# Optimization experiments

Hardware: AMD Instinct MI355X
Metric: run time of the kernel (lower is better)

## Reference

```python
import jax, jax.numpy as jnp
import numpy as np

N_HEADS = 8  # must match init_kwargs n_heads


def _shift(x, dy, dx):
    """out[..., y, x] = x[..., y+dy, x+dx], zero-padded outside. Replaces im2col gather / col2im scatter."""
    H, W = x.shape[-2], x.shape[-1]
    py0, py1 = max(dy, 0), max(-dy, 0)
    px0, px1 = max(dx, 0), max(-dx, 0)
    xp = jnp.pad(x, [(0, 0)] * (x.ndim - 2) + [(py1, py0), (px1, px0)])
    return xp[..., py1 + dy:py1 + dy + H, px1 + dx:px1 + dx + W]


def setup_inputs() -> dict:
    key = jax.random.key(0)
    k1, k2, k3 = jax.random.split(key, 3)
    N, D, H, W = 8, 256, 128, 128
    V = jax.random.normal(k1, (N, D, H, W), dtype=jnp.float32)
    K = jax.random.normal(k2, (N, D, H, W), dtype=jnp.float32)
    Q = jax.random.normal(k3, (N, D, H, W), dtype=jnp.float32)
    mask = jnp.ones((N, 1, H, W), dtype=jnp.float32)
    return {"V": V, "K": K, "Q": Q, "ksize": 5, "dilation": 1, "mask": mask}


def reference(V, K, Q, ksize, dilation, mask):
    N, D, H, W = Q.shape
    Dv = V.shape[1]
    nh = N_HEADS
    h_dim = D // nh
    dv_h = Dv // nh
    pad = (ksize // 2) * dilation
    offsets = [(i * dilation - pad, j * dilation - pad)
               for i in range(ksize) for j in range(ksize)]  # P = ksize**2 window positions

    # per-head QK scores for each window offset: score_p = sum_c K[y+dy, x+dx] * Q[y, x]
    Qh = Q.reshape(N, nh, h_dim, H, W)
    scores = []
    for (dy, dx) in offsets:
        Ks = _shift(K, dy, dx).reshape(N, nh, h_dim, H, W)
        scores.append(jnp.sum(Ks * Qh, axis=2))  # (N, nh, H, W)
    scores = jnp.stack(scores, axis=0)  # (P, N, nh, H, W)

    # softmax over window positions (dim 2 in the torch code), then mask
    att = jax.nn.softmax(scores, axis=0)
    m = mask.reshape(N, 1, H, W)[:, 0]  # (N, H, W)
    att = att * m[None, :, None, :, :]

    # diffuse V: value at (y, x) weighted by att[p] scatters to (y+dy, x+dx) (col2im add)
    Vh = V.reshape(N, nh, dv_h, H, W)
    out = jnp.zeros((N, nh, dv_h, H, W), dtype=V.dtype)
    for p, (dy, dx) in enumerate(offsets):
        contrib = Vh * att[p][:, :, None]  # (N, nh, dv_h, H, W)
        out = out + _shift(contrib, -dy, -dx)
    return out.reshape(N, Dv, H, W)
```

## Files before the change

### kernel.cpp

```cpp
#include <hip/hip_runtime.h>
#include <hip/hip_bf16.h>

typedef __hip_bfloat16 bf16;

#define N_     8
#define NH     8
#define HD     32
#define HW     (128 * 128)
#define H_     128
#define W_     128
#define P_     25
#define TY     8
#define RG     12
#define PITCH  136
#define CH     4
#define NCH    (HD / CH)
#define NPLANE (N_ * NH * HW)

static __device__ __forceinline__ unsigned short f2bf(float f) {
  bf16 b = __float2bfloat16(f);
  return *(unsigned short*)&b;
}

__global__ __launch_bounds__(512) void attn_kernel(
    const float* __restrict__ Kp, const float* __restrict__ Qp,
    const float* __restrict__ maskp, bf16* __restrict__ att) {
  __shared__ float L[CH][RG][PITCH];

  const int tid = threadIdx.x;
  const int y0 = blockIdx.x * TY, nh = blockIdx.y;
  const int ty = tid >> 6, g = tid & 63;
  const int gy = y0 + ty, gx0 = 2 * g;
  const float* KU = Kp + (size_t)nh * (HD * HW);
  const float* QU = Qp + (size_t)nh * (HD * HW);

  const int scol = tid & 127;
  const int sr0  = tid >> 7;
  int gofs[3]; bool okr[3];
#pragma unroll
  for (int j = 0; j < 3; ++j) {
    const int ky = y0 - 2 + sr0 + 4 * j;
    okr[j] = (unsigned)ky < H_;
    gofs[j] = okr[j] ? ky * W_ + scol : 0;
  }

  if (tid < 192) {
    const int ch = tid / 48, rem = tid % 48, r = rem >> 2, c = rem & 3;
    L[ch][r][c < 2 ? c : c + 128] = 0.f;
  }

  float s[P_][2];
#pragma unroll
  for (int p = 0; p < P_; ++p) { s[p][0] = 0.f; s[p][1] = 0.f; }

  float t[3][CH];
#pragma unroll
  for (int j = 0; j < 3; ++j)
#pragma unroll
    for (int ch = 0; ch < CH; ++ch)
      t[j][ch] = okr[j] ? KU[gofs[j] + ch * HW] : 0.f;

#pragma unroll 1
  for (int kc = 0; kc < NCH; ++kc) {
    const int c0 = kc * CH;
    float q[CH][2];
#pragma unroll
    for (int ch = 0; ch < CH; ++ch) {
      float2 qv = *(const float2*)(QU + (c0 + ch) * HW + gy * W_ + gx0);
      q[ch][0] = qv.x; q[ch][1] = qv.y;
    }

    if (kc) __syncthreads();
#pragma unroll
    for (int j = 0; j < 3; ++j)
#pragma unroll
      for (int ch = 0; ch < CH; ++ch)
        L[ch][sr0 + 4 * j][scol + 2] = t[j][ch];
    __syncthreads();

    if (kc < NCH - 1) {
      const int cn = (kc + 1) * CH;
#pragma unroll
      for (int j = 0; j < 3; ++j)
#pragma unroll
        for (int ch = 0; ch < CH; ++ch)
          t[j][ch] = okr[j] ? KU[gofs[j] + (cn + ch) * HW] : 0.f;
    }

#pragma unroll
    for (int ch = 0; ch < CH; ++ch)
#pragma unroll
      for (int dyi = 0; dyi < 5; ++dyi) {
        const float* rp = &L[ch][ty + dyi][2 * g];
        float2 ra = *(const float2*)rp;
        float2 rb = *(const float2*)(rp + 2);
        float2 rc = *(const float2*)(rp + 4);
        float r[6] = {ra.x, ra.y, rb.x, rb.y, rc.x, rc.y};
#pragma unroll
        for (int dxi = 0; dxi < 5; ++dxi) {
          s[dyi * 5 + dxi][0] += r[0 + dxi] * q[ch][0];
          s[dyi * 5 + dxi][1] += r[1 + dxi] * q[ch][1];
        }
      }
  }

  float2 mv = *(const float2*)(maskp + (size_t)(nh >> 3) * HW + gy * W_ + gx0);
  float inv[2];
#pragma unroll
  for (int px = 0; px < 2; ++px) {
    float m = s[0][px];
#pragma unroll
    for (int p = 1; p < P_; ++p) m = fmaxf(m, s[p][px]);
    float sum = 0.f;
#pragma unroll
    for (int p = 0; p < P_; ++p) { float e = __expf(s[p][px] - m); s[p][px] = e; sum += e; }
    inv[px] = (px ? mv.y : mv.x) / sum;
  }
  unsigned short* A = (unsigned short*)att;
  const size_t pixbase = (size_t)nh * HW + gy * W_ + gx0;
#pragma unroll
  for (int p = 0; p < P_; ++p) {
    unsigned o = (unsigned)f2bf(s[p][0] * inv[0]) |
                 ((unsigned)f2bf(s[p][1] * inv[1]) << 16);
    *(unsigned*)(A + (size_t)p * NPLANE + pixbase) = o;
  }
}

__global__ __launch_bounds__(256) void diffuse_kernel(
    const float* __restrict__ Vp, const bf16* __restrict__ att,
    float* __restrict__ out) {
  __shared__ float L[CH][RG][PITCH];

  const int tid = threadIdx.x;
  const int y0 = blockIdx.x * TY, nh = blockIdx.y;
  const int ty = tid >> 5, g = tid & 31;
  const int gy = y0 + ty, gx0 = 4 * g;
  const float* VU = Vp + (size_t)nh * (HD * HW);
  float* OU = out + (size_t)nh * (HD * HW);

  const int scol = tid & 127;
  const int sr0  = tid >> 7;
  int gofs[6]; bool okr[6];
#pragma unroll
  for (int j = 0; j < 6; ++j) {
    const int ky = y0 - 2 + sr0 + 2 * j;
    okr[j] = (unsigned)ky < H_;
    gofs[j] = okr[j] ? ky * W_ + scol : 0;
  }

  float t[6][CH];
#pragma unroll
  for (int j = 0; j < 6; ++j)
#pragma unroll
    for (int ch = 0; ch < CH; ++ch)
      t[j][ch] = okr[j] ? VU[gofs[j] + ch * HW] : 0.f;

  const unsigned short* A = (const unsigned short*)att;
  unsigned mxl[5], mxh[5];
#pragma unroll
  for (int exi = 0; exi < 5; ++exi) {
    bool o0 = (unsigned)(gx0 + 0 + exi - 2) < W_;
    bool o1 = (unsigned)(gx0 + 1 + exi - 2) < W_;
    bool o2 = (unsigned)(gx0 + 2 + exi - 2) < W_;
    bool o3 = (unsigned)(gx0 + 3 + exi - 2) < W_;
    mxl[exi] = (o0 ? 0xFFFFu : 0u) | (o1 ? 0xFFFF0000u : 0u);
    mxh[exi] = (o2 ? 0xFFFFu : 0u) | (o3 ? 0xFFFF0000u : 0u);
  }
  uint2 wp[P_];
#pragma unroll
  for (int j = 0; j < P_; ++j) {
    const int eyi = j / 5, exi = j % 5;
    const int ys = gy + eyi - 2;
    uint2 v; v.x = 0u; v.y = 0u;
    if ((unsigned)ys < H_) {
      const size_t base = (size_t)(24 - j) * NPLANE + (size_t)nh * HW +
                          (size_t)(ys * W_) + (gx0 + exi - 2);
      if (exi == 2) {
        v = *(const uint2*)(A + base);
      } else if ((exi & 1) == 0) {
        v.x = *(const unsigned*)(A + base);
        v.y = *(const unsigned*)(A + base + 2);
      } else {
        unsigned u0 = *(const unsigned*)(A + base - 1);
        unsigned u1 = *(const unsigned*)(A + base + 1);
        unsigned u2 = *(const unsigned*)(A + base + 3);
        v.x = (u0 >> 16) | (u1 << 16);
        v.y = (u1 >> 16) | (u2 << 16);
      }
    }
    v.x &= mxl[exi]; v.y &= mxh[exi];
    wp[j] = v;
  }

  if (tid < 192) {
    const int ch = tid / 48, rem = tid % 48, r = rem >> 2, c = rem & 3;
    L[ch][r][c < 2 ? c : c + 128] = 0.f;
  }

#pragma unroll 1
  for (int kc = 0; kc < NCH; ++kc) {
    if (kc) __syncthreads();
#pragma unroll
    for (int j = 0; j < 6; ++j)
#pragma unroll
      for (int ch = 0; ch < CH; ++ch)
        L[ch][sr0 + 2 * j][scol + 2] = t[j][ch];
    __syncthreads();

    if (kc < NCH - 1) {
      const int cn = (kc + 1) * CH;
#pragma unroll
      for (int j = 0; j < 6; ++j)
#pragma unroll
        for (int ch = 0; ch < CH; ++ch)
          t[j][ch] = okr[j] ? VU[gofs[j] + (cn + ch) * HW] : 0.f;
    }

    float acc[CH][4];
#pragma unroll
    for (int ch = 0; ch < CH; ++ch)
#pragma unroll
      for (int px = 0; px < 4; ++px) acc[ch][px] = 0.f;

#pragma unroll
    for (int eyi = 0; eyi < 5; ++eyi) {
      float vr[CH][8];
#pragma unroll
      for (int ch = 0; ch < CH; ++ch) {
        const float* rp = &L[ch][ty + eyi][4 * g];
        float4 ra = *(const float4*)rp;
        float4 rb = *(const float4*)(rp + 4);
        vr[ch][0] = ra.x; vr[ch][1] = ra.y; vr[ch][2] = ra.z; vr[ch][3] = ra.w;
        vr[ch][4] = rb.x; vr[ch][5] = rb.y; vr[ch][6] = rb.z; vr[ch][7] = rb.w;
      }
#pragma unroll
      for (int exi = 0; exi < 5; ++exi) {
        const uint2 w2 = wp[eyi * 5 + exi];
        float wf[4];
        wf[0] = __uint_as_float(w2.x << 16);
        wf[1] = __uint_as_float(w2.x & 0xFFFF0000u);
        wf[2] = __uint_as_float(w2.y << 16);
        wf[3] = __uint_as_float(w2.y & 0xFFFF0000u);
#pragma unroll
        for (int ch = 0; ch < CH; ++ch)
#pragma unroll
          for (int px = 0; px < 4; ++px)
            acc[ch][px] += wf[px] * vr[ch][px + exi];
      }
    }

    const int c0 = kc * CH;
#pragma unroll
    for (int ch = 0; ch < CH; ++ch) {
      float4 o = make_float4(acc[ch][0], acc[ch][1], acc[ch][2], acc[ch][3]);
      *(float4*)(OU + (c0 + ch) * HW + gy * W_ + gx0) = o;
    }
  }
}

extern "C" void kernel_launch(void* const* d_in, const int* in_sizes, int n_in,
                              void* d_out, int out_size, void* d_ws, size_t ws_size,
                              hipStream_t stream) {
  const float* V    = (const float*)d_in[0];
  const float* K    = (const float*)d_in[1];
  const float* Q    = (const float*)d_in[2];
  const float* mask = (const float*)d_in[5];

  bf16* att = (bf16*)d_ws;

  dim3 grid(H_ / TY, N_ * NH);
  attn_kernel<<<grid, 512, 0, stream>>>(K, Q, mask, att);
  diffuse_kernel<<<grid, 256, 0, stream>>>(V, att, (float*)d_out);
}
```

Baseline: 170.5 us.

## Load K window directly from global memory in attention kernel, drop LDS staging

Measured after the change: 312.5 us. +83.3%, slower.

```diff
diff --git a/kernel.cpp b/kernel.cpp
--- a/kernel.cpp
+++ b/kernel.cpp
@@ -10,98 +10,95 @@
 #define H_     128
 #define W_     128
 #define P_     25
+#define CH     4
+#define NCH    (HD / CH)
+#define NPLANE (N_ * NH * HW)
+
 #define TY     8
 #define RG     12
 #define PITCH  136
-#define CH     4
-#define NCH    (HD / CH)
-#define NPLANE (N_ * NH * HW)
+
+#define ATY    4
 
 static __device__ __forceinline__ unsigned short f2bf(float f) {
   bf16 b = __float2bfloat16(f);
   return *(unsigned short*)&b;
 }
 
-__global__ __launch_bounds__(512) void attn_kernel(
+__global__ __launch_bounds__(256) void attn_kernel(
     const float* __restrict__ Kp, const float* __restrict__ Qp,
     const float* __restrict__ maskp, bf16* __restrict__ att) {
-  __shared__ float L[CH][RG][PITCH];
-
   const int tid = threadIdx.x;
-  const int y0 = blockIdx.x * TY, nh = blockIdx.y;
+  const int y0 = blockIdx.x * ATY, nh = blockIdx.y;
   const int ty = tid >> 6, g = tid & 63;
   const int gy = y0 + ty, gx0 = 2 * g;
   const float* KU = Kp + (size_t)nh * (HD * HW);
   const float* QU = Qp + (size_t)nh * (HD * HW);
 
-  const int scol = tid & 127;
-  const int sr0  = tid >> 7;
-  int gofs[3]; bool okr[3];
-#pragma unroll
-  for (int j = 0; j < 3; ++j) {
-    const int ky = y0 - 2 + sr0 + 4 * j;
-    okr[j] = (unsigned)ky < H_;
-    gofs[j] = okr[j] ? ky * W_ + scol : 0;
-  }
-
-  if (tid < 192) {
-    const int ch = tid / 48, rem = tid % 48, r = rem >> 2, c = rem & 3;
-    L[ch][r][c < 2 ? c : c + 128] = 0.f;
-  }
+  int rowoff[5]; bool rowok[5];
+#pragma unroll
+  for (int d = 0; d < 5; ++d) {
+    const int yy = gy + d - 2;
+    rowok[d] = (unsigned)yy < H_;
+    const int yc = yy < 0 ? 0 : (yy > H_ - 1 ? H_ - 1 : yy);
+    rowoff[d] = yc * W_;
+  }
+  const int c0 = (g == 0) ? 0 : (2 * g - 2);
+  const int c1 = 2 * g;
+  const int c2 = (g == 63) ? 124 : (2 * g + 2);
 
   float s[P_][2];
 #pragma unroll
   for (int p = 0; p < P_; ++p) { s[p][0] = 0.f; s[p][1] = 0.f; }
-
-  float t[3][CH];
-#pragma unroll
-  for (int j = 0; j < 3; ++j)
-#pragma unroll
-    for (int ch = 0; ch < CH; ++ch)
-      t[j][ch] = okr[j] ? KU[gofs[j] + ch * HW] : 0.f;
 
 #pragma unroll 1
   for (int kc = 0; kc < NCH; ++kc) {
-    const int c0 = kc * CH;
+    const int cb = kc * CH;
     float q[CH][2];
 #pragma unroll
     for (int ch = 0; ch < CH; ++ch) {
-      float2 qv = *(const float2*)(QU + (c0 + ch) * HW + gy * W_ + gx0);
+      float2 qv = *(const float2*)(QU + (cb + ch) * HW + gy * W_ + gx0);
       q[ch][0] = qv.x; q[ch][1] = qv.y;
     }
 
-    if (kc) __syncthreads();
-#pragma unroll
-    for (int j = 0; j < 3; ++j)
-#pragma unroll
-      for (int ch = 0; ch < CH; ++ch)
-        L[ch][sr0 + 4 * j][scol + 2] = t[j][ch];
-    __syncthreads();
-
-    if (kc < NCH - 1) {
-      const int cn = (kc + 1) * CH;
-#pragma unroll
-      for (int j = 0; j < 3; ++j)
-#pragma unroll
-        for (int ch = 0; ch < CH; ++ch)
-          t[j][ch] = okr[j] ? KU[gofs[j] + (cn + ch) * HW] : 0.f;
-    }
-
-#pragma unroll
-    for (int ch = 0; ch < CH; ++ch)
-#pragma unroll
-      for (int dyi = 0; dyi < 5; ++dyi) {
-        const float* rp = &L[ch][ty + dyi][2 * g];
-        float2 ra = *(const float2*)rp;
-        float2 rb = *(const float2*)(rp + 2);
-        float2 rc = *(const float2*)(rp + 4);
-        float r[6] = {ra.x, ra.y, rb.x, rb.y, rc.x, rc.y};
+#pragma unroll
+    for (int ch = 0; ch < CH; ++ch) {
+      const float* Kc = KU + (cb + ch) * HW;
+#pragma unroll
+      for (int d = 0; d < 5; ++d) {
+        const float* kr = Kc + rowoff[d];
+        float2 ra = *(const float2*)(kr + c0);
+        float2 rb = *(const float2*)(kr + c1);
+        float2 rc = *(const float2*)(kr + c2);
+        const float r[6] = {ra.x, ra.y, rb.x, rb.y, rc.x, rc.y};
 #pragma unroll
         for (int dxi = 0; dxi < 5; ++dxi) {
-          s[dyi * 5 + dxi][0] += r[0 + dxi] * q[ch][0];
-          s[dyi * 5 + dxi][1] += r[1 + dxi] * q[ch][1];
+          s[d * 5 + dxi][0] += r[0 + dxi] * q[ch][0];
+          s[d * 5 + dxi][1] += r[1 + dxi] * q[ch][1];
         }
       }
+    }
+  }
+
+#pragma unroll
+  for (int d = 0; d < 5; ++d)
+    if (!rowok[d]) {
+#pragma unroll
+      for (int dxi = 0; dxi < 5; ++dxi) { s[d * 5 + dxi][0] = 0.f; s[d * 5 + dxi][1] = 0.f; }
+    }
+  if (g == 0) {
+#pragma unroll
+    for (int d = 0; d < 5; ++d) {
+      s[d * 5 + 0][0] = 0.f; s[d * 5 + 1][0] = 0.f;
+      s[d * 5 + 0][1] = 0.f;
+    }
+  }
+  if (g == 63) {
+#pragma unroll
+    for (int d = 0; d < 5; ++d) {
+      s[d * 5 + 4][0] = 0.f;
+      s[d * 5 + 3][1] = 0.f; s[d * 5 + 4][1] = 0.f;
+    }
   }
 
   float2 mv = *(const float2*)(maskp + (size_t)(nh >> 3) * HW + gy * W_ + gx0);
@@ -268,7 +265,8 @@
 
   bf16* att = (bf16*)d_ws;
 
-  dim3 grid(H_ / TY, N_ * NH);
-  attn_kernel<<<grid, 512, 0, stream>>>(K, Q, mask, att);
-  diffuse_kernel<<<grid, 256, 0, stream>>>(V, att, (float*)d_out);
-}
+  dim3 gridA(H_ / ATY, N_ * NH);
+  attn_kernel<<<gridA, 256, 0, stream>>>(K, Q, mask, att);
+  dim3 gridB(H_ / TY, N_ * NH);
+  diffuse_kernel<<<gridB, 256, 0, stream>>>(V, att, (float*)d_out);
+}
```
